# Kernel optimization log

Measured on AMD Instinct MI355X. Metric: run time of the kernel, lower is better.

## Reference

```python
import jax, jax.numpy as jnp
import numpy as np

B = 2            # batch size
NPB = 49152      # voxels per batch (multiple of GROUP -> padding path is identity)
N = B * NPB
C = 128          # embed_dim
HEADS = 8
GROUP = 128      # group_size
WIN = 12         # win_size
SY, SX = 468, 468  # sparse_shape (y, x)
GD = C // 4      # per-branch channels in CWI_FFN
CONV = WIN + 1   # conv_size = 13


def _bn(x, g, b):
    # training-mode BatchNorm1d, eps=1e-3, biased variance
    m = x.mean(0)
    v = x.var(0)
    return (x - m) * jax.lax.rsqrt(v + 1e-3) * g + b


def _subm_conv(f, w, dense, coords):
    # submanifold sparse 2D conv: output only at active sites, gather active neighbors
    Ky, Kx = w.shape[0], w.shape[1]
    cb, cy, cx = coords[:, 0], coords[:, 1], coords[:, 2]
    out = jnp.zeros((f.shape[0], w.shape[3]), f.dtype)
    for ky in range(Ky):
        for kx in range(Kx):
            ny = cy + (ky - Ky // 2)
            nx = cx + (kx - Kx // 2)
            valid = (ny >= 0) & (ny < SY) & (nx >= 0) & (nx < SX)
            nidx = dense[cb, jnp.clip(ny, 0, SY - 1), jnp.clip(nx, 0, SX - 1)]
            valid = valid & (nidx >= 0)
            nb = jnp.where(valid[:, None], f[jnp.clip(nidx, 0)], 0.0)
            out = out + nb @ w[ky, kx]
    return out


def setup_inputs() -> dict:
    rng = np.random.default_rng(0)
    cs = []
    for b in range(B):
        flat = rng.choice(SY * SX, NPB, replace=False)  # unique voxels per batch
        cs.append(np.stack([np.full(NPB, b), flat // SX, flat % SX], 1))
    coords = jnp.asarray(np.concatenate(cs, 0).astype(np.int32))
    key = jax.random.key(0)
    ks = jax.random.split(key, 10)
    s = lambda k, shape, fan: jax.random.normal(k, shape, jnp.float32) / np.sqrt(fan)
    return dict(
        feats=jax.random.normal(ks[0], (N, C), jnp.float32),
        coords=coords,
        qkv_w=s(ks[1], (C, 3 * C), C),
        fc_out_w=s(ks[2], (C, C), C), fc_out_b=jnp.zeros((C,), jnp.float32),
        norm0_g=jnp.ones((C,), jnp.float32), norm0_b=jnp.zeros((C,), jnp.float32),
        bn1_g=jnp.ones((C,), jnp.float32), bn1_b=jnp.zeros((C,), jnp.float32),
        bn2_g=jnp.ones((C,), jnp.float32), bn2_b=jnp.zeros((C,), jnp.float32),
        convk_w=s(ks[3], (3, 3, GD, GD), 9 * GD),
        convh_w=s(ks[4], (1, CONV, GD, GD), CONV * GD),
        convw_w=s(ks[5], (CONV, 1, GD, GD), CONV * GD),
        fc1_w=s(ks[6], (C, 2 * C), C), fc1_b=jnp.zeros((2 * C,), jnp.float32),
        fc2_w=s(ks[7], (2 * C, C), 2 * C), fc2_b=jnp.zeros((C,), jnp.float32),
    )


def reference(feats, coords, qkv_w, fc_out_w, fc_out_b, norm0_g, norm0_b,
              bn1_g, bn1_b, bn2_g, bn2_b, convk_w, convh_w, convw_w,
              fc1_w, fc1_b, fc2_w, fc2_b):
    # --- FlattenedWindowMapping, direction 'x' (module returns after 1st direction) ---
    mwx = int(np.ceil(SX / WIN)) + 1
    mwy = int(np.ceil(SY / WIN)) + 1
    per = mwx * mwy
    cb = coords[:, 0].astype(jnp.int64)
    cy = coords[:, 1].astype(jnp.int64)
    cx = coords[:, 2].astype(jnp.int64)
    win_id_x = cb * per + (cx // WIN) * mwy + (cy // WIN)
    vx = win_id_x * (WIN * WIN) + (cx % WIN) * WIN + (cy % WIN)  # unique per voxel
    idx = jnp.argsort(vx)
    # counts per batch divide GROUP -> flat2win / win2flat are identity

    # --- grouped multi-head attention ---
    xf = _bn(feats[idx], norm0_g, norm0_b)
    q, k, v = jnp.split(xf @ qkv_w, 3, axis=1)
    ng = N // GROUP
    hd = C // HEADS
    r = lambda t: t.reshape(ng, GROUP, HEADS, hd).transpose(0, 2, 1, 3)  # (n,h,g,d)
    q, k, v = r(q), r(k), r(v)
    att = jax.nn.softmax(jnp.einsum('nhqd,nhkd->nhqk', q, k) / np.sqrt(C), axis=-1)
    out = jnp.einsum('nhqk,nhkd->nhqd', att, v).transpose(0, 2, 1, 3).reshape(N, C)
    out = out @ fc_out_w + fc_out_b
    feats = feats.at[idx].add(out)  # idx is a permutation: residual + scatter-back

    # --- CWI FFN ---
    dense = jnp.full((B, SY, SX), -1, jnp.int32).at[
        coords[:, 0], coords[:, 1], coords[:, 2]].set(jnp.arange(N, dtype=jnp.int32))
    srcn = _bn(feats, bn1_g, bn1_b)
    sk = _subm_conv(srcn[:, :GD], convk_w, dense, coords)
    sh = _subm_conv(srcn[:, GD:2 * GD], convh_w, dense, coords)
    sw = _subm_conv(srcn[:, 2 * GD:3 * GD], convw_w, dense, coords)
    src2 = jnp.concatenate([sk, sh, sw, srcn[:, 3 * GD:]], 1)
    src = srcn + src2
    src2 = jax.nn.relu(_bn(src, bn2_g, bn2_b) @ fc1_w + fc1_b) @ fc2_w + fc2_b
    return src + src2
```

## Files before the change

### kernel.cpp

```cpp
#include <hip/hip_runtime.h>

#define N_PTS 98304
#define SY 468
#define SX 468
#define WIN 12
#define MWY 40
#define PER 1600
#define NWIN 3200
#define NSLOT (NWIN*144)
#define NDENSE (2*SY*SX)
#define CPB 32

using bf16x8 = __attribute__((ext_vector_type(8))) short;
using bf16x4 = __attribute__((ext_vector_type(4))) short;
using f32x4  = __attribute__((ext_vector_type(4))) float;

__device__ __forceinline__ unsigned short f2bf(float f){
  unsigned u = __float_as_uint(f);
  u += 0x7fffu + ((u>>16)&1u);
  return (unsigned short)(u>>16);
}
__device__ __forceinline__ float2 bfp2(unsigned u){
  float2 r; r.x = __uint_as_float(u<<16); r.y = __uint_as_float(u & 0xffff0000u); return r;
}
__device__ __forceinline__ unsigned fpack2(float a, float b){
  return (unsigned)f2bf(a) | ((unsigned)f2bf(b)<<16);
}

__device__ __forceinline__ f32x4 mfma16(bf16x4 a, bf16x4 b, f32x4 c){
#if __has_builtin(__builtin_amdgcn_mfma_f32_16x16x16bf16_1k)
  return __builtin_amdgcn_mfma_f32_16x16x16bf16_1k(a, b, c, 0, 0, 0);
#else
  asm volatile("v_mfma_f32_16x16x16_bf16 %0, %1, %2, %0\n\ts_nop 7\n\ts_nop 7"
               : "+v"(c) : "v"(a), "v"(b));
  return c;
#endif
}

constexpr size_t OFF_SORTED = 0;
constexpr size_t OFF_SLOT   = OFF_SORTED + (size_t)N_PTS*4;
constexpr size_t OFF_CNT    = OFF_SLOT + (size_t)NSLOT*4;
constexpr size_t OFF_OFFS   = OFF_CNT + (size_t)NWIN*4;
constexpr size_t OFF_STATS  = OFF_OFFS + (size_t)NWIN*4;
constexpr size_t OFF_SB     = OFF_STATS + 3*256*4;
constexpr size_t OFF_BQKV   = OFF_SB + 3*256*4;
constexpr size_t OFF_B1     = OFF_BQKV + 512*4;
constexpr size_t OFF_WQKV   = OFF_B1 + 256*4;
constexpr size_t OFF_WOUT   = OFF_WQKV + (size_t)128*384*2;
constexpr size_t OFF_W1     = OFF_WOUT + (size_t)128*128*2;
constexpr size_t OFF_W2     = OFF_W1 + (size_t)128*256*2;
constexpr size_t OFF_WCONV  = OFF_W2 + (size_t)256*128*2;
constexpr size_t OFF_DENSE  = OFF_WCONV + (size_t)35*1024*2;
constexpr size_t OFF_QKV    = (OFF_DENSE + (size_t)NDENSE*4 + 255) & ~(size_t)255;
constexpr size_t OFF_SRC    = OFF_QKV;
constexpr size_t OFF_SRCB   = OFF_QKV + (size_t)N_PTS*128*4;
constexpr size_t OFF_ATT    = OFF_QKV + (size_t)N_PTS*384*2;
constexpr size_t OFF_SRCNB  = OFF_ATT;
constexpr size_t OFF_F2     = OFF_ATT + (size_t)N_PTS*128*2;
constexpr size_t OFF_H      = OFF_F2;

__global__ void fill_i32(int* p, int v, int n){
  int i = blockIdx.x*256 + threadIdx.x;
  if (i < n) p[i] = v;
}

__global__ void keys_kernel(const int* __restrict__ coords, int* __restrict__ slot){
  int i = blockIdx.x*256 + threadIdx.x;
  if (i >= N_PTS) return;
  int cb = coords[3*i], cy = coords[3*i+1], cx = coords[3*i+2];
  int w = cb*PER + (cx/WIN)*MWY + (cy/WIN);
  int sub = (cx%WIN)*WIN + (cy%WIN);
  slot[w*144 + sub] = i;
}

__global__ void wincount_kernel(const int* __restrict__ slot, int* __restrict__ cnt){
  int w = blockIdx.x*256 + threadIdx.x;
  if (w >= NWIN) return;
  int c = 0;
  for (int s = 0; s < 144; ++s) c += (slot[w*144+s] >= 0);
  cnt[w] = c;
}

__global__ void scan_kernel(const int* __restrict__ cnt, int* __restrict__ offs){
  __shared__ int tsum[256];
  int tid = threadIdx.x;
  int loc[13]; int s = 0;
  #pragma unroll
  for (int j = 0; j < 13; ++j){
    int idx = tid*13 + j;
    int v = (idx < NWIN) ? cnt[idx] : 0;
    loc[j] = s; s += v;
  }
  tsum[tid] = s;
  __syncthreads();
  for (int off = 1; off < 256; off <<= 1){
    int v = (tid >= off) ? tsum[tid-off] : 0;
    __syncthreads();
    tsum[tid] += v;
    __syncthreads();
  }
  int pre = (tid > 0) ? tsum[tid-1] : 0;
  #pragma unroll
  for (int j = 0; j < 13; ++j){
    int idx = tid*13 + j;
    if (idx < NWIN) offs[idx] = pre + loc[j];
  }
}

__global__ void scatter_kernel(const int* __restrict__ slot, const int* __restrict__ offs,
                               int* __restrict__ sorted){
  int w = blockIdx.x*256 + threadIdx.x;
  if (w >= NWIN) return;
  int o = offs[w];
  for (int s = 0; s < 144; ++s){
    int v = slot[w*144+s];
    if (v >= 0) sorted[o++] = v;
  }
}

__global__ void dense_kernel(const int* __restrict__ coords, int* __restrict__ dense){
  int i = blockIdx.x*256 + threadIdx.x;
  if (i >= N_PTS) return;
  dense[(coords[3*i]*SY + coords[3*i+1])*SX + coords[3*i+2]] = i;
}

__global__ __launch_bounds__(256) void bnstats_kernel(const float* __restrict__ x, float* __restrict__ stats){
  __shared__ float sh[256], shq[256];
  int tid = threadIdx.x;
  int c = tid & 127;
  float s = 0.f, q = 0.f;
  for (int r = blockIdx.x*2 + (tid>>7); r < N_PTS; r += gridDim.x*2){
    float v = x[(size_t)r*128 + c];
    s += v; q += v*v;
  }
  sh[tid] = s; shq[tid] = q;
  __syncthreads();
  if (tid < 128){
    atomicAdd(&stats[tid],     sh[tid] + sh[tid+128]);
    atomicAdd(&stats[128+tid], shq[tid] + shq[tid+128]);
  }
}

__global__ void bnfinish_kernel(const float* __restrict__ stats, const float* __restrict__ g,
                                const float* __restrict__ b, float* __restrict__ sb){
  int c = threadIdx.x;
  if (c >= 128) return;
  float mean = stats[c] * (1.0f/N_PTS);
  float var  = stats[128+c] * (1.0f/N_PTS) - mean*mean;
  float s = g[c] * rsqrtf(var + 1e-3f);
  sb[c] = s;
  sb[128+c] = b[c] - mean*s;
}

__global__ void packw_kernel(const float* __restrict__ W, const float* __restrict__ scale,
                             short* __restrict__ out, int K, int Nn){
  int t = blockIdx.x*256 + threadIdx.x;
  if (t >= K*Nn) return;
  int e = t & 7, l = (t>>3) & 63, jt = (t>>9) & 7;
  int rest = t >> 12;
  int KT = K >> 5;
  int kt = rest % KT, np = rest / KT;
  int k = kt*32 + ((l>>4)<<3) + e;
  int col = np*128 + jt*16 + (l&15);
  float v = W[(size_t)k*Nn + col];
  if (scale) v *= scale[k];
  out[t] = (short)f2bf(v);
}

__global__ void packbias_kernel(const float* __restrict__ W, const float* __restrict__ bvec,
                                const float* __restrict__ base, float* __restrict__ out, int K, int Nn){
  int o = blockIdx.x*256 + threadIdx.x;
  if (o >= Nn) return;
  float s = base ? base[o] : 0.f;
  for (int k = 0; k < K; ++k) s += bvec[k] * W[(size_t)k*Nn + o];
  out[o] = s;
}

__global__ void packconv_kernel(const float* __restrict__ wk, const float* __restrict__ wh,
                                const float* __restrict__ ww, short* __restrict__ out){
  int t = blockIdx.x*256 + threadIdx.x;
  if (t >= 35*2*64*8) return;
  int e = t & 7, l = (t>>3) & 63, jt = (t>>9) & 1, tap = t >> 10;
  int ci = ((l>>4)<<3) + e;
  int co = jt*16 + (l&15);
  float v;
  if (tap < 9)       v = wk[((size_t)(tap*32) + ci)*32 + co];
  else if (tap < 22) v = wh[((size_t)((tap-9)*32) + ci)*32 + co];
  else               v = ww[((size_t)((tap-22)*32) + ci)*32 + co];
  out[t] = (short)f2bf(v);
}

__global__ __launch_bounds__(256) void srcn_kernel(const float* __restrict__ f2, const float* __restrict__ sb,
                            short* __restrict__ sbuf){
  size_t i = (size_t)blockIdx.x*256 + threadIdx.x;
  if (i >= (size_t)N_PTS*32) return;
  int c4 = ((int)(i & 31)) * 4;
  float4 v = ((const float4*)f2)[i];
  float4 o;
  o.x = v.x*sb[c4+0] + sb[128+c4+0];
  o.y = v.y*sb[c4+1] + sb[128+c4+1];
  o.z = v.z*sb[c4+2] + sb[128+c4+2];
  o.w = v.w*sb[c4+3] + sb[128+c4+3];
  uint2 h; h.x = fpack2(o.x, o.y); h.y = fpack2(o.z, o.w);
  ((uint2*)sbuf)[i] = h;
}

template<int K, int AMODE, int EPI>
__global__ __launch_bounds__(256) void gemm_kernel(
    const float* __restrict__ Afp, const short* __restrict__ Abf,
    const int* __restrict__ sorted, const short* __restrict__ Wp,
    const float* __restrict__ bias, const float* __restrict__ addf,
    float* __restrict__ outf, short* __restrict__ outb, float* __restrict__ stats,
    int dstStride)
{
  extern __shared__ char smem[];
  const int m0 = blockIdx.x * 128;
  const int np = blockIdx.y;
  const int tid = threadIdx.x;
  if (AMODE == 0){
    const int CHK = K/4;
    for (int c = tid; c < 128*CHK; c += 256){
      int r = c / CHK, q = c % CHK;
      const float* arow = Afp + (size_t)sorted[m0+r]*K;
      float4 v = ((const float4*)arow)[q];
      int off = r*(K*2) + q*8; off ^= ((r&7)<<4);
      *reinterpret_cast<uint2*>(smem+off) = make_uint2(fpack2(v.x,v.y), fpack2(v.z,v.w));
    }
  } else {
    const int CHK = K/8;
    for (int c = tid; c < 128*CHK; c += 256){
      int r = c / CHK, q = c % CHK;
      uint4 v = ((const uint4*)(Abf + (size_t)(m0+r)*K))[q];
      int off = r*(K*2) + q*16; off ^= ((r&7)<<4);
      *reinterpret_cast<uint4*>(smem+off) = v;
    }
  }
  __syncthreads();
  const int w = tid >> 6, l = tid & 63, lg = l >> 4, l16 = l & 15;
  f32x4 zacc; zacc[0]=0.f; zacc[1]=0.f; zacc[2]=0.f; zacc[3]=0.f;
  f32x4 acc[2][8];
  #pragma unroll
  for (int mt=0; mt<2; ++mt)
    #pragma unroll
    for (int jt=0; jt<8; ++jt) acc[mt][jt] = zacc;
  const int KT = K/32;
  #pragma unroll
  for (int kt = 0; kt < KT; ++kt){
    const short* wk = Wp + ((size_t)(np*KT + kt))*4096;
    bf16x8 bfr[8];
    #pragma unroll
    for (int jt=0; jt<8; ++jt)
      bfr[jt] = *reinterpret_cast<const bf16x8*>(wk + jt*512 + l*8);
    #pragma unroll
    for (int mt=0; mt<2; ++mt){
      int row = w*32 + mt*16 + l16;
      int off = row*(K*2) + kt*64 + lg*16; off ^= ((row&7)<<4);
      bf16x8 af = *reinterpret_cast<const bf16x8*>(smem + off);
      #pragma unroll
      for (int jt=0; jt<8; ++jt)
        acc[mt][jt] = __builtin_amdgcn_mfma_f32_16x16x32_bf16(af, bfr[jt], acc[mt][jt], 0, 0, 0);
    }
  }
  float psum[8], psq[8];
  #pragma unroll
  for (int jt=0; jt<8; ++jt){ psum[jt]=0.f; psq[jt]=0.f; }
  #pragma unroll
  for (int mt=0; mt<2; ++mt){
    #pragma unroll
    for (int jt=0; jt<8; ++jt){
      int col = np*128 + jt*16 + l16;
      float bv = bias ? bias[col] : 0.f;
      #pragma unroll
      for (int e=0; e<4; ++e){
        int row = m0 + w*32 + mt*16 + lg*4 + e;
        float v = acc[mt][jt][e] + bv;
        if (EPI == 0){
          outb[(size_t)row*dstStride + col] = (short)f2bf(v);
        } else if (EPI == 1){
          int gi = sorted[row];
          float fv = addf[(size_t)gi*128 + col] + v;
          outf[(size_t)gi*128 + col] = fv;
          psum[jt] += fv; psq[jt] += fv*fv;
        } else if (EPI == 2){
          outb[(size_t)row*dstStride + col] = (short)f2bf(fmaxf(v, 0.f));
        } else if (EPI == 3){
          outf[(size_t)row*128 + col] = addf[(size_t)row*128 + col] + v;
        } else {
          int r = row - m0;
          int blk = (m0 >> 7)*24 + np*8 + jt;
          outb[(size_t)blk*2048 + r*16 + l16] = (short)f2bf(v);
        }
      }
    }
  }
  if (EPI == 1){
    __syncthreads();
    float* cs = (float*)smem;
    cs[tid] = 0.f;
    __syncthreads();
    float* cq = cs + 128;
    #pragma unroll
    for (int jt=0; jt<8; ++jt){
      atomicAdd(&cs[jt*16 + l16], psum[jt]);
      atomicAdd(&cq[jt*16 + l16], psq[jt]);
    }
    __syncthreads();
    if (tid < 128){
      atomicAdd(&stats[tid],     cs[tid]);
      atomicAdd(&stats[128+tid], cq[tid]);
    }
  }
}

__global__ __launch_bounds__(256) void attn_kernel(const short* __restrict__ qkv, short* __restrict__ attout){
  __shared__ char VT[8192];
  const int g = blockIdx.x;
  const int hp = blockIdx.y;
  const int tid = threadIdx.x;
  const short* gb = qkv + (size_t)g*24*2048;
  for (int c = tid; c < 512; c += 256){
    int hh = c >> 8, idx = c & 255, token = idx >> 1, q = idx & 1;
    uint4 v = *(const uint4*)(gb + (16 + 2*hp + hh)*2048 + token*16 + q*8);
    const unsigned short* hv = (const unsigned short*)&v;
    #pragma unroll
    for (int j = 0; j < 8; ++j){
      int ch = hh*16 + q*8 + j;
      int F = ((ch & 7) ^ ((ch >> 3) & 7)) << 4;
      *(unsigned short*)(VT + ch*256 + ((token*2) ^ F)) = hv[j];
    }
  }
  __syncthreads();
  const int w = tid>>6, l = tid&63, lg = l>>4, l16 = l&15;
  const float sc2 = 0.12751744f;
  f32x4 z4; z4[0]=0.f; z4[1]=0.f; z4[2]=0.f; z4[3]=0.f;
  #pragma unroll
  for (int hh = 0; hh < 2; ++hh){
    const int h = 2*hp + hh;
    const short* Qb = gb + h*2048;
    const short* Kb = gb + (8 + h)*2048;
    bf16x4 qf0 = *(const bf16x4*)(Qb + (w*32      + l16)*16 + lg*4);
    bf16x4 qf1 = *(const bf16x4*)(Qb + (w*32 + 16 + l16)*16 + lg*4);
    f32x4 s[8][2];
    #pragma unroll
    for (int kb=0; kb<8; ++kb){ s[kb][0] = z4; s[kb][1] = z4; }
    #pragma unroll
    for (int kb=0; kb<8; ++kb){
      bf16x4 kf = *(const bf16x4*)(Kb + (kb*16 + l16)*16 + lg*4);
      s[kb][0] = mfma16(kf, qf0, s[kb][0]);
      s[kb][1] = mfma16(kf, qf1, s[kb][1]);
    }
    float inv0, inv1;
    #pragma unroll
    for (int mt=0; mt<2; ++mt){
      float m = -1e30f;
      #pragma unroll
      for (int kb=0; kb<8; ++kb)
        #pragma unroll
        for (int e=0; e<4; ++e) m = fmaxf(m, s[kb][mt][e]);
      m = fmaxf(m, __shfl_xor(m, 16));
      m = fmaxf(m, __shfl_xor(m, 32));
      float d = 0.f;
      #pragma unroll
      for (int kb=0; kb<8; ++kb)
        #pragma unroll
        for (int e=0; e<4; ++e){
          float p = exp2f((s[kb][mt][e] - m) * sc2);
          s[kb][mt][e] = p; d += p;
        }
      d += __shfl_xor(d, 16);
      d += __shfl_xor(d, 32);
      if (mt == 0) inv0 = 1.0f/d; else inv1 = 1.0f/d;
    }
    f32x4 o0 = z4, o1 = z4;
    const int cc = hh*16 + l16;
    const int F = ((cc & 7) ^ ((cc >> 3) & 7)) << 4;
    #pragma unroll
    for (int kb=0; kb<8; ++kb){
      bf16x4 vb = *(const bf16x4*)(VT + cc*256 + ((kb*32 + lg*8) ^ F));
      bf16x4 pa0, pa1;
      #pragma unroll
      for (int e=0; e<4; ++e){
        pa0[e] = (short)f2bf(s[kb][0][e] * inv0);
        pa1[e] = (short)f2bf(s[kb][1][e] * inv1);
      }
      o0 = mfma16(pa0, vb, o0);
      o1 = mfma16(pa1, vb, o1);
    }
    #pragma unroll
    for (int e=0; e<4; ++e){
      int row0 = g*128 + w*32      + lg*4 + e;
      int row1 = g*128 + w*32 + 16 + lg*4 + e;
      attout[(size_t)row0*128 + h*16 + l16] = (short)f2bf(o0[e]);
      attout[(size_t)row1*128 + h*16 + l16] = (short)f2bf(o1[e]);
    }
  }
}

template<int G>
__global__ __launch_bounds__(256) void conv_kernel(
    const short* __restrict__ wfrag, const short* __restrict__ srcnb,
    const int* __restrict__ dense, const int* __restrict__ coords,
    float* __restrict__ src)
{
  constexpr int TC   = (G==0) ? 9 : 13;
  constexpr int TAP0 = (G==0) ? 0 : ((G==1) ? 9 : 22);
  __shared__ int scoords[CPB*3];
  __shared__ int nid[CPB*16];
  extern __shared__ char nbf[];
  const int tid = threadIdx.x;
  const int p0 = blockIdx.x * CPB;
  if (tid < CPB*3) scoords[tid] = coords[p0*3 + tid];
  const int w = tid>>6, l = tid&63, lg = l>>4, l16 = l&15;
  const int mt = w & 1, jt = w >> 1;
  bf16x8 bw[TC];
  #pragma unroll
  for (int t = 0; t < TC; ++t)
    bw[t] = *reinterpret_cast<const bf16x8*>(wfrag + (((TAP0+t)*2 + jt)*64 + l)*8);
  __syncthreads();
  for (int i = tid; i < TC*CPB; i += 256){
    int tap = i >> 5, p = i & 31;
    int cb = scoords[p*3], cy = scoords[p*3+1], cx = scoords[p*3+2];
    int dy, dx;
    if (G==0){ dy = tap/3 - 1; dx = tap%3 - 1; }
    else if (G==1){ dy = 0; dx = tap - 6; }
    else { dy = tap - 6; dx = 0; }
    int ny = cy+dy, nx = cx+dx;
    int v = -1;
    if (ny>=0 && ny<SY && nx>=0 && nx<SX) v = dense[(cb*SY+ny)*SX + nx];
    nid[p*16 + tap] = v;
  }
  __syncthreads();
  for (int i = tid; i < TC*CPB*4; i += 256){
    int c = i & 3, s = i >> 2;
    int tap = s >> 5, p = s & 31;
    int v = nid[p*16 + tap];
    uint4 val = make_uint4(0,0,0,0);
    if (v >= 0) val = *(const uint4*)(srcnb + (size_t)v*128 + G*32 + c*8);
    int off = (tap*CPB + p)*80 + ((c*16) ^ ((p&3)<<4));
    *(uint4*)(nbf + off) = val;
  }
  __syncthreads();
  f32x4 acc; acc[0]=0.f; acc[1]=0.f; acc[2]=0.f; acc[3]=0.f;
  const int pA = mt*16 + l16;
  #pragma unroll
  for (int t = 0; t < TC; ++t){
    int off = (t*CPB + pA)*80 + ((lg*16) ^ ((pA&3)<<4));
    bf16x8 af = *reinterpret_cast<const bf16x8*>(nbf + off);
    acc = __builtin_amdgcn_mfma_f32_16x16x32_bf16(af, bw[t], acc, 0, 0, 0);
  }
  #pragma unroll
  for (int e = 0; e < 4; ++e){
    int pi = p0 + mt*16 + lg*4 + e;
    int c = G*32 + jt*16 + l16;
    unsigned short rv = ((const unsigned short*)srcnb)[(size_t)pi*128 + c];
    src[(size_t)pi*128 + c] = __uint_as_float((unsigned)rv << 16) + acc[e];
  }
}

__global__ __launch_bounds__(256) void post_kernel(float* __restrict__ src, const short* __restrict__ srcnb,
                           short* __restrict__ srcb, float* __restrict__ stats){
  __shared__ float ss[128], sq[128];
  int tid = threadIdx.x;
  if (tid < 128){ ss[tid]=0.f; sq[tid]=0.f; }
  __syncthreads();
  int c4 = (tid & 31) * 4;
  float a0=0,a1=0,a2=0,a3=0, q0=0,q1=0,q2=0,q3=0;
  for (int r = blockIdx.x*8 + (tid>>5); r < N_PTS; r += gridDim.x*8){
    size_t base = (size_t)r*128 + c4;
    float4 v;
    if (c4 < 96){
      v = *(const float4*)(src + base);
    } else {
      uint2 sn = *(const uint2*)(srcnb + base);
      float2 p0 = bfp2(sn.x), p1 = bfp2(sn.y);
      v = make_float4(2.f*p0.x, 2.f*p0.y, 2.f*p1.x, 2.f*p1.y);
      *(float4*)(src + base) = v;
    }
    uint2 h; h.x = fpack2(v.x, v.y); h.y = fpack2(v.z, v.w);
    *(uint2*)(srcb + base) = h;
    a0+=v.x; a1+=v.y; a2+=v.z; a3+=v.w;
    q0+=v.x*v.x; q1+=v.y*v.y; q2+=v.z*v.z; q3+=v.w*v.w;
  }
  atomicAdd(&ss[c4+0],a0); atomicAdd(&ss[c4+1],a1); atomicAdd(&ss[c4+2],a2); atomicAdd(&ss[c4+3],a3);
  atomicAdd(&sq[c4+0],q0); atomicAdd(&sq[c4+1],q1); atomicAdd(&sq[c4+2],q2); atomicAdd(&sq[c4+3],q3);
  __syncthreads();
  if (tid < 128){
    atomicAdd(&stats[tid],     ss[tid]);
    atomicAdd(&stats[128+tid], sq[tid]);
  }
}

extern "C" void kernel_launch(void* const* d_in, const int* in_sizes, int n_in,
                              void* d_out, int out_size, void* d_ws, size_t ws_size,
                              hipStream_t stream)
{
  const float* feats    = (const float*)d_in[0];
  const int*   coords   = (const int*)d_in[1];
  const float* qkv_w    = (const float*)d_in[2];
  const float* fc_out_w = (const float*)d_in[3];
  const float* fc_out_b = (const float*)d_in[4];
  const float* norm0_g  = (const float*)d_in[5];
  const float* norm0_b  = (const float*)d_in[6];
  const float* bn1_g    = (const float*)d_in[7];
  const float* bn1_b    = (const float*)d_in[8];
  const float* bn2_g    = (const float*)d_in[9];
  const float* bn2_b    = (const float*)d_in[10];
  const float* convk_w  = (const float*)d_in[11];
  const float* convh_w  = (const float*)d_in[12];
  const float* convw_w  = (const float*)d_in[13];
  const float* fc1_w    = (const float*)d_in[14];
  const float* fc1_b    = (const float*)d_in[15];
  const float* fc2_w    = (const float*)d_in[16];
  const float* fc2_b    = (const float*)d_in[17];
  float* out = (float*)d_out;
  char* ws = (char*)d_ws;

  int*   sorted = (int*)(ws + OFF_SORTED);
  int*   slot   = (int*)(ws + OFF_SLOT);
  int*   cnt    = (int*)(ws + OFF_CNT);
  int*   offs   = (int*)(ws + OFF_OFFS);
  float* stats0 = (float*)(ws + OFF_STATS);
  float* stats1 = stats0 + 256;
  float* stats2 = stats0 + 512;
  float* sb0    = (float*)(ws + OFF_SB);
  float* sb1    = sb0 + 256;
  float* sb2    = sb0 + 512;
  float* bqkv   = (float*)(ws + OFF_BQKV);
  float* b1     = (float*)(ws + OFF_B1);
  short* wqkv   = (short*)(ws + OFF_WQKV);
  short* wout   = (short*)(ws + OFF_WOUT);
  short* w1     = (short*)(ws + OFF_W1);
  short* w2     = (short*)(ws + OFF_W2);
  short* wconv  = (short*)(ws + OFF_WCONV);
  int*   dense  = (int*)(ws + OFF_DENSE);
  short* qkvb   = (short*)(ws + OFF_QKV);
  float* srcf   = (float*)(ws + OFF_SRC);
  short* srcb   = (short*)(ws + OFF_SRCB);
  short* att    = (short*)(ws + OFF_ATT);
  short* srcnb  = (short*)(ws + OFF_SRCNB);
  float* feats2 = (float*)(ws + OFF_F2);
  short* Hbuf   = (short*)(ws + OFF_H);

  fill_i32<<<(NSLOT+255)/256, 256, 0, stream>>>(slot, -1, NSLOT);
  fill_i32<<<(NDENSE+255)/256, 256, 0, stream>>>(dense, -1, NDENSE);
  fill_i32<<<3, 256, 0, stream>>>((int*)stats0, 0, 768);

  keys_kernel<<<(N_PTS+255)/256, 256, 0, stream>>>(coords, slot);
  wincount_kernel<<<(NWIN+255)/256, 256, 0, stream>>>(slot, cnt);
  scan_kernel<<<1, 256, 0, stream>>>(cnt, offs);
  scatter_kernel<<<(NWIN+255)/256, 256, 0, stream>>>(slot, offs, sorted);
  dense_kernel<<<(N_PTS+255)/256, 256, 0, stream>>>(coords, dense);

  bnstats_kernel<<<512, 256, 0, stream>>>(feats, stats0);
  bnfinish_kernel<<<1, 128, 0, stream>>>(stats0, norm0_g, norm0_b, sb0);
  packw_kernel<<<(128*384+255)/256, 256, 0, stream>>>(qkv_w, sb0, wqkv, 128, 384);
  packbias_kernel<<<2, 256, 0, stream>>>(qkv_w, sb0+128, nullptr, bqkv, 128, 384);
  packw_kernel<<<(128*128+255)/256, 256, 0, stream>>>(fc_out_w, nullptr, wout, 128, 128);

  gemm_kernel<128,0,4><<<dim3(768,3), 256, 32768, stream>>>(feats, nullptr, sorted, wqkv, bqkv, nullptr, nullptr, qkvb, nullptr, 0);
  attn_kernel<<<dim3(768,4), 256, 0, stream>>>(qkvb, att);
  gemm_kernel<128,1,1><<<dim3(768,1), 256, 32768, stream>>>(nullptr, att, sorted, wout, fc_out_b, feats, feats2, nullptr, stats1, 128);

  bnfinish_kernel<<<1, 128, 0, stream>>>(stats1, bn1_g, bn1_b, sb1);
  srcn_kernel<<<(N_PTS*32+255)/256, 256, 0, stream>>>(feats2, sb1, srcnb);

  packconv_kernel<<<(35*2*64*8+255)/256, 256, 0, stream>>>(convk_w, convh_w, convw_w, wconv);
  conv_kernel<0><<<N_PTS/CPB, 256,  9*CPB*80, stream>>>(wconv, srcnb, dense, coords, srcf);
  conv_kernel<1><<<N_PTS/CPB, 256, 13*CPB*80, stream>>>(wconv, srcnb, dense, coords, srcf);
  conv_kernel<2><<<N_PTS/CPB, 256, 13*CPB*80, stream>>>(wconv, srcnb, dense, coords, srcf);
  post_kernel<<<512, 256, 0, stream>>>(srcf, srcnb, srcb, stats2);
  bnfinish_kernel<<<1, 128, 0, stream>>>(stats2, bn2_g, bn2_b, sb2);

  packw_kernel<<<(128*256+255)/256, 256, 0, stream>>>(fc1_w, sb2, w1, 128, 256);
  packbias_kernel<<<1, 256, 0, stream>>>(fc1_w, sb2+128, fc1_b, b1, 128, 256);
  packw_kernel<<<(256*128+255)/256, 256, 0, stream>>>(fc2_w, nullptr, w2, 256, 128);

  gemm_kernel<128,1,2><<<dim3(768,2), 256, 32768, stream>>>(nullptr, srcb, nullptr, w1, b1, nullptr, nullptr, Hbuf, nullptr, 256);
  gemm_kernel<256,1,3><<<dim3(768,1), 256, 65536, stream>>>(nullptr, Hbuf, nullptr, w2, fc2_b, srcf, out, nullptr, nullptr, 128);

  (void)in_sizes; (void)n_in; (void)out_size; (void)ws_size;
}
```

Measured before the change: 611.8 us.

## Work in window-sorted order with a pre-gathered bf16 feature copy throughout

A gather kernel first copies features into window-sorted order as bf16, together with their coordinates. Every later stage then runs in sorted order: BN stats read bf16, the QKV GEMM reads contiguous rows and handles all three output slices in one block, and the residual feats2 is stored as bf16. The scatter back to the original order happens only in the final FFN GEMM epilogue. This removes the random-access gathers and scatters in the middle of the pipeline and halves the bytes of several fp32 passes, but the residual path now loses precision to bf16.

After: 572.8 us. -6.4%, faster.

```diff
diff --git a/kernel.cpp b/kernel.cpp
--- a/kernel.cpp
+++ b/kernel.cpp
@@ -51,7 +51,9 @@
 constexpr size_t OFF_W2     = OFF_W1 + (size_t)128*256*2;
 constexpr size_t OFF_WCONV  = OFF_W2 + (size_t)256*128*2;
 constexpr size_t OFF_DENSE  = OFF_WCONV + (size_t)35*1024*2;
-constexpr size_t OFF_QKV    = (OFF_DENSE + (size_t)NDENSE*4 + 255) & ~(size_t)255;
+constexpr size_t OFF_CORS   = OFF_DENSE + (size_t)NDENSE*4;
+constexpr size_t OFF_FB     = (OFF_CORS + (size_t)N_PTS*12 + 255) & ~(size_t)255;
+constexpr size_t OFF_QKV    = (OFF_FB + (size_t)N_PTS*128*2 + 255) & ~(size_t)255;
 constexpr size_t OFF_SRC    = OFF_QKV;
 constexpr size_t OFF_SRCB   = OFF_QKV + (size_t)N_PTS*128*4;
 constexpr size_t OFF_ATT    = OFF_QKV + (size_t)N_PTS*384*2;
@@ -118,26 +120,57 @@
   }
 }
 
-__global__ void dense_kernel(const int* __restrict__ coords, int* __restrict__ dense){
+__global__ __launch_bounds__(256) void gather_kernel(const float* __restrict__ feats,
+    const int* __restrict__ coords, const int* __restrict__ sorted,
+    short* __restrict__ featsb, int* __restrict__ coordsS){
+  int t = blockIdx.x*256 + threadIdx.x;
+  if (t >= N_PTS*32) return;
+  int row = t >> 5, q = t & 31;
+  int src = sorted[row];
+  float4 v = ((const float4*)(feats + (size_t)src*128))[q];
+  uint2 h; h.x = fpack2(v.x, v.y); h.y = fpack2(v.z, v.w);
+  ((uint2*)featsb)[t] = h;
+  if (q == 0){
+    coordsS[3*row+0] = coords[3*src+0];
+    coordsS[3*row+1] = coords[3*src+1];
+    coordsS[3*row+2] = coords[3*src+2];
+  }
+}
+
+__global__ void dense_kernel(const int* __restrict__ coordsS, int* __restrict__ dense){
   int i = blockIdx.x*256 + threadIdx.x;
   if (i >= N_PTS) return;
-  dense[(coords[3*i]*SY + coords[3*i+1])*SX + coords[3*i+2]] = i;
-}
-
-__global__ __launch_bounds__(256) void bnstats_kernel(const float* __restrict__ x, float* __restrict__ stats){
-  __shared__ float sh[256], shq[256];
+  dense[(coordsS[3*i]*SY + coordsS[3*i+1])*SX + coordsS[3*i+2]] = i;
+}
+
+__global__ __launch_bounds__(256) void bnstatsb_kernel(const short* __restrict__ x, float* __restrict__ stats){
+  __shared__ float ss[128], sq[128];
   int tid = threadIdx.x;
-  int c = tid & 127;
-  float s = 0.f, q = 0.f;
-  for (int r = blockIdx.x*2 + (tid>>7); r < N_PTS; r += gridDim.x*2){
-    float v = x[(size_t)r*128 + c];
-    s += v; q += v*v;
-  }
-  sh[tid] = s; shq[tid] = q;
+  if (tid < 128){ ss[tid]=0.f; sq[tid]=0.f; }
+  __syncthreads();
+  int c8 = (tid & 15) * 8;
+  float a[8], q[8];
+  #pragma unroll
+  for (int j=0;j<8;++j){ a[j]=0.f; q[j]=0.f; }
+  for (int r = blockIdx.x*16 + (tid>>4); r < N_PTS; r += gridDim.x*16){
+    uint4 v = *(const uint4*)(x + (size_t)r*128 + c8);
+    const unsigned* wv = (const unsigned*)&v;
+    #pragma unroll
+    for (int k=0;k<4;++k){
+      float2 p = bfp2(wv[k]);
+      a[2*k]   += p.x; q[2*k]   += p.x*p.x;
+      a[2*k+1] += p.y; q[2*k+1] += p.y*p.y;
+    }
+  }
+  #pragma unroll
+  for (int j=0;j<8;++j){
+    atomicAdd(&ss[c8+j], a[j]);
+    atomicAdd(&sq[c8+j], q[j]);
+  }
   __syncthreads();
   if (tid < 128){
-    atomicAdd(&stats[tid],     sh[tid] + sh[tid+128]);
-    atomicAdd(&stats[128+tid], shq[tid] + shq[tid+128]);
+    atomicAdd(&stats[tid],     ss[tid]);
+    atomicAdd(&stats[128+tid], sq[tid]);
   }
 }
 
@@ -190,26 +223,79 @@
   out[t] = (short)f2bf(v);
 }
 
-__global__ __launch_bounds__(256) void srcn_kernel(const float* __restrict__ f2, const float* __restrict__ sb,
+__global__ __launch_bounds__(256) void srcnb_kernel(const short* __restrict__ f2, const float* __restrict__ sb,
                             short* __restrict__ sbuf){
-  size_t i = (size_t)blockIdx.x*256 + threadIdx.x;
-  if (i >= (size_t)N_PTS*32) return;
-  int c4 = ((int)(i & 31)) * 4;
-  float4 v = ((const float4*)f2)[i];
-  float4 o;
-  o.x = v.x*sb[c4+0] + sb[128+c4+0];
-  o.y = v.y*sb[c4+1] + sb[128+c4+1];
-  o.z = v.z*sb[c4+2] + sb[128+c4+2];
-  o.w = v.w*sb[c4+3] + sb[128+c4+3];
-  uint2 h; h.x = fpack2(o.x, o.y); h.y = fpack2(o.z, o.w);
+  int i = blockIdx.x*256 + threadIdx.x;
+  if (i >= N_PTS*32) return;
+  int c4 = (i & 31) * 4;
+  uint2 v = ((const uint2*)f2)[i];
+  float2 p0 = bfp2(v.x), p1 = bfp2(v.y);
+  float o0 = p0.x*sb[c4+0] + sb[128+c4+0];
+  float o1 = p0.y*sb[c4+1] + sb[128+c4+1];
+  float o2 = p1.x*sb[c4+2] + sb[128+c4+2];
+  float o3 = p1.y*sb[c4+3] + sb[128+c4+3];
+  uint2 h; h.x = fpack2(o0, o1); h.y = fpack2(o2, o3);
   ((uint2*)sbuf)[i] = h;
 }
 
-template<int K, int AMODE, int EPI>
+__global__ __launch_bounds__(256) void qkvgemm_kernel(const short* __restrict__ Abf,
+    const short* __restrict__ Wp, const float* __restrict__ bias, short* __restrict__ outb){
+  __shared__ char smem[32768];
+  const int m0 = blockIdx.x * 128;
+  const int tid = threadIdx.x;
+  for (int c = tid; c < 128*16; c += 256){
+    int r = c >> 4, q = c & 15;
+    uint4 v = ((const uint4*)(Abf + (size_t)(m0+r)*128))[q];
+    int off = r*256 + q*16; off ^= ((r&7)<<4);
+    *reinterpret_cast<uint4*>(smem+off) = v;
+  }
+  __syncthreads();
+  const int w = tid>>6, l = tid&63, lg = l>>4, l16 = l&15;
+  f32x4 zacc; zacc[0]=0.f; zacc[1]=0.f; zacc[2]=0.f; zacc[3]=0.f;
+  for (int np = 0; np < 3; ++np){
+    f32x4 acc[2][8];
+    #pragma unroll
+    for (int mt=0; mt<2; ++mt)
+      #pragma unroll
+      for (int jt=0; jt<8; ++jt) acc[mt][jt] = zacc;
+    #pragma unroll
+    for (int kt = 0; kt < 4; ++kt){
+      const short* wk = Wp + ((size_t)(np*4 + kt))*4096;
+      bf16x8 bfr[8];
+      #pragma unroll
+      for (int jt=0; jt<8; ++jt)
+        bfr[jt] = *reinterpret_cast<const bf16x8*>(wk + jt*512 + l*8);
+      #pragma unroll
+      for (int mt=0; mt<2; ++mt){
+        int row = w*32 + mt*16 + l16;
+        int off = row*256 + kt*64 + lg*16; off ^= ((row&7)<<4);
+        bf16x8 af = *reinterpret_cast<const bf16x8*>(smem + off);
+        #pragma unroll
+        for (int jt=0; jt<8; ++jt)
+          acc[mt][jt] = __builtin_amdgcn_mfma_f32_16x16x32_bf16(af, bfr[jt], acc[mt][jt], 0, 0, 0);
+      }
+    }
+    #pragma unroll
+    for (int mt=0; mt<2; ++mt){
+      #pragma unroll
+      for (int jt=0; jt<8; ++jt){
+        float bv = bias[np*128 + jt*16 + l16];
+        int blk = blockIdx.x*24 + np*8 + jt;
+        #pragma unroll
+        for (int e=0; e<4; ++e){
+          int r = w*32 + mt*16 + lg*4 + e;
+          outb[(size_t)blk*2048 + r*16 + l16] = (short)f2bf(acc[mt][jt][e] + bv);
+        }
+      }
+    }
+  }
+}
+
+template<int K, int EPI>
 __global__ __launch_bounds__(256) void gemm_kernel(
-    const float* __restrict__ Afp, const short* __restrict__ Abf,
-    const int* __restrict__ sorted, const short* __restrict__ Wp,
-    const float* __restrict__ bias, const float* __restrict__ addf,
+    const short* __restrict__ Abf, const int* __restrict__ sorted,
+    const short* __restrict__ Wp, const float* __restrict__ bias,
+    const short* __restrict__ addb, const float* __restrict__ addf,
     float* __restrict__ outf, short* __restrict__ outb, float* __restrict__ stats,
     int dstStride)
 {
@@ -217,23 +303,12 @@
   const int m0 = blockIdx.x * 128;
   const int np = blockIdx.y;
   const int tid = threadIdx.x;
-  if (AMODE == 0){
-    const int CHK = K/4;
-    for (int c = tid; c < 128*CHK; c += 256){
-      int r = c / CHK, q = c % CHK;
-      const float* arow = Afp + (size_t)sorted[m0+r]*K;
-      float4 v = ((const float4*)arow)[q];
-      int off = r*(K*2) + q*8; off ^= ((r&7)<<4);
-      *reinterpret_cast<uint2*>(smem+off) = make_uint2(fpack2(v.x,v.y), fpack2(v.z,v.w));
-    }
-  } else {
-    const int CHK = K/8;
-    for (int c = tid; c < 128*CHK; c += 256){
-      int r = c / CHK, q = c % CHK;
-      uint4 v = ((const uint4*)(Abf + (size_t)(m0+r)*K))[q];
-      int off = r*(K*2) + q*16; off ^= ((r&7)<<4);
-      *reinterpret_cast<uint4*>(smem+off) = v;
-    }
+  const int CHK = K/8;
+  for (int c = tid; c < 128*CHK; c += 256){
+    int r = c / CHK, q = c % CHK;
+    uint4 v = ((const uint4*)(Abf + (size_t)(m0+r)*K))[q];
+    int off = r*(K*2) + q*16; off ^= ((r&7)<<4);
+    *reinterpret_cast<uint4*>(smem+off) = v;
   }
   __syncthreads();
   const int w = tid >> 6, l = tid & 63, lg = l >> 4, l16 = l & 15;
@@ -274,21 +349,15 @@
       for (int e=0; e<4; ++e){
         int row = m0 + w*32 + mt*16 + lg*4 + e;
         float v = acc[mt][jt][e] + bv;
-        if (EPI == 0){
-          outb[(size_t)row*dstStride + col] = (short)f2bf(v);
-        } else if (EPI == 1){
-          int gi = sorted[row];
-          float fv = addf[(size_t)gi*128 + col] + v;
-          outf[(size_t)gi*128 + col] = fv;
+        if (EPI == 1){
+          unsigned short rb = ((const unsigned short*)addb)[(size_t)row*128 + col];
+          float fv = __uint_as_float((unsigned)rb << 16) + v;
+          outb[(size_t)row*128 + col] = (short)f2bf(fv);
           psum[jt] += fv; psq[jt] += fv*fv;
         } else if (EPI == 2){
           outb[(size_t)row*dstStride + col] = (short)f2bf(fmaxf(v, 0.f));
-        } else if (EPI == 3){
-          outf[(size_t)row*128 + col] = addf[(size_t)row*128 + col] + v;
         } else {
-          int r = row - m0;
-          int blk = (m0 >> 7)*24 + np*8 + jt;
-          outb[(size_t)blk*2048 + r*16 + l16] = (short)f2bf(v);
+          outf[(size_t)sorted[row]*128 + col] = addf[(size_t)row*128 + col] + v;
         }
       }
     }
@@ -399,7 +468,7 @@
 template<int G>
 __global__ __launch_bounds__(256) void conv_kernel(
     const short* __restrict__ wfrag, const short* __restrict__ srcnb,
-    const int* __restrict__ dense, const int* __restrict__ coords,
+    const int* __restrict__ dense, const int* __restrict__ coordsS,
     float* __restrict__ src)
 {
   constexpr int TC   = (G==0) ? 9 : 13;
@@ -409,7 +478,7 @@
   extern __shared__ char nbf[];
   const int tid = threadIdx.x;
   const int p0 = blockIdx.x * CPB;
-  if (tid < CPB*3) scoords[tid] = coords[p0*3 + tid];
+  if (tid < CPB*3) scoords[tid] = coordsS[p0*3 + tid];
   const int w = tid>>6, l = tid&63, lg = l>>4, l16 = l&15;
   const int mt = w & 1, jt = w >> 1;
   bf16x8 bw[TC];
@@ -533,12 +602,14 @@
   short* w2     = (short*)(ws + OFF_W2);
   short* wconv  = (short*)(ws + OFF_WCONV);
   int*   dense  = (int*)(ws + OFF_DENSE);
+  int*   coordsS= (int*)(ws + OFF_CORS);
+  short* featsb = (short*)(ws + OFF_FB);
   short* qkvb   = (short*)(ws + OFF_QKV);
   float* srcf   = (float*)(ws + OFF_SRC);
   short* srcb   = (short*)(ws + OFF_SRCB);
   short* att    = (short*)(ws + OFF_ATT);
   short* srcnb  = (short*)(ws + OFF_SRCNB);
-  float* feats2 = (float*)(ws + OFF_F2);
+  short* feats2 = (short*)(ws + OFF_F2);
   short* Hbuf   = (short*)(ws + OFF_H);
 
   fill_i32<<<(NSLOT+255)/256, 256, 0, stream>>>(slot, -1, NSLOT);
@@ -549,25 +620,26 @@
   wincount_kernel<<<(NWIN+255)/256, 256, 0, stream>>>(slot, cnt);
   scan_kernel<<<1, 256, 0, stream>>>(cnt, offs);
   scatter_kernel<<<(NWIN+255)/256, 256, 0, stream>>>(slot, offs, sorted);
-  dense_kernel<<<(N_PTS+255)/256, 256, 0, stream>>>(coords, dense);
-
-  bnstats_kernel<<<512, 256, 0, stream>>>(feats, stats0);
+  gather_kernel<<<(N_PTS*32+255)/256, 256, 0, stream>>>(feats, coords, sorted, featsb, coordsS);
+  dense_kernel<<<(N_PTS+255)/256, 256, 0, stream>>>(coordsS, dense);
+
+  bnstatsb_kernel<<<512, 256, 0, stream>>>(featsb, stats0);
   bnfinish_kernel<<<1, 128, 0, stream>>>(stats0, norm0_g, norm0_b, sb0);
   packw_kernel<<<(128*384+255)/256, 256, 0, stream>>>(qkv_w, sb0, wqkv, 128, 384);
   packbias_kernel<<<2, 256, 0, stream>>>(qkv_w, sb0+128, nullptr, bqkv, 128, 384);
   packw_kernel<<<(128*128+255)/256, 256, 0, stream>>>(fc_out_w, nullptr, wout, 128, 128);
 
-  gemm_kernel<128,0,4><<<dim3(768,3), 256, 32768, stream>>>(feats, nullptr, sorted, wqkv, bqkv, nullptr, nullptr, qkvb, nullptr, 0);
+  qkvgemm_kernel<<<768, 256, 0, stream>>>(featsb, wqkv, bqkv, qkvb);
   attn_kernel<<<dim3(768,4), 256, 0, stream>>>(qkvb, att);
-  gemm_kernel<128,1,1><<<dim3(768,1), 256, 32768, stream>>>(nullptr, att, sorted, wout, fc_out_b, feats, feats2, nullptr, stats1, 128);
+  gemm_kernel<128,1><<<dim3(768,1), 256, 32768, stream>>>(att, nullptr, wout, fc_out_b, featsb, nullptr, nullptr, feats2, stats1, 128);
 
   bnfinish_kernel<<<1, 128, 0, stream>>>(stats1, bn1_g, bn1_b, sb1);
-  srcn_kernel<<<(N_PTS*32+255)/256, 256, 0, stream>>>(feats2, sb1, srcnb);
+  srcnb_kernel<<<(N_PTS*32+255)/256, 256, 0, stream>>>(feats2, sb1, srcnb);
 
   packconv_kernel<<<(35*2*64*8+255)/256, 256, 0, stream>>>(convk_w, convh_w, convw_w, wconv);
-  conv_kernel<0><<<N_PTS/CPB, 256,  9*CPB*80, stream>>>(wconv, srcnb, dense, coords, srcf);
-  conv_kernel<1><<<N_PTS/CPB, 256, 13*CPB*80, stream>>>(wconv, srcnb, dense, coords, srcf);
-  conv_kernel<2><<<N_PTS/CPB, 256, 13*CPB*80, stream>>>(wconv, srcnb, dense, coords, srcf);
+  conv_kernel<0><<<N_PTS/CPB, 256,  9*CPB*80, stream>>>(wconv, srcnb, dense, coordsS, srcf);
+  conv_kernel<1><<<N_PTS/CPB, 256, 13*CPB*80, stream>>>(wconv, srcnb, dense, coordsS, srcf);
+  conv_kernel<2><<<N_PTS/CPB, 256, 13*CPB*80, stream>>>(wconv, srcnb, dense, coordsS, srcf);
   post_kernel<<<512, 256, 0, stream>>>(srcf, srcnb, srcb, stats2);
   bnfinish_kernel<<<1, 128, 0, stream>>>(stats2, bn2_g, bn2_b, sb2);
 
@@ -575,8 +647,8 @@
   packbias_kernel<<<1, 256, 0, stream>>>(fc1_w, sb2+128, fc1_b, b1, 128, 256);
   packw_kernel<<<(256*128+255)/256, 256, 0, stream>>>(fc2_w, nullptr, w2, 256, 128);
 
-  gemm_kernel<128,1,2><<<dim3(768,2), 256, 32768, stream>>>(nullptr, srcb, nullptr, w1, b1, nullptr, nullptr, Hbuf, nullptr, 256);
-  gemm_kernel<256,1,3><<<dim3(768,1), 256, 65536, stream>>>(nullptr, Hbuf, nullptr, w2, fc2_b, srcf, out, nullptr, nullptr, 128);
+  gemm_kernel<128,2><<<dim3(768,2), 256, 32768, stream>>>(srcb, nullptr, w1, b1, nullptr, nullptr, nullptr, Hbuf, nullptr, 256);
+  gemm_kernel<256,5><<<dim3(768,1), 256, 65536, stream>>>(Hbuf, sorted, w2, fc2_b, nullptr, srcf, out, nullptr, nullptr, 128);
 
   (void)in_sizes; (void)n_in; (void)out_size; (void)ws_size;
 }
```
